# Kernel optimization log

Measured on AMD Instinct MI355X. Metric: run time of the kernel, lower is better.

Reference implementation:

```python
import jax, jax.numpy as jnp
import numpy as np

PADDING_IDX = 0
N_WORDS = 256  # max_n_words (num_segments for pooling)


def _segment_mean(h, wid):
    # h: (S, H), wid: (S,) int32 in [0, N_WORDS). Mean-pool subwords per word.
    sums = jax.ops.segment_sum(h, wid, num_segments=N_WORDS)          # (W, H)
    cnt = jax.ops.segment_sum(jnp.ones(wid.shape, h.dtype), wid,
                              num_segments=N_WORDS)                    # (W,)
    # words with no subwords -> zero vector (matches pad_sequence padding_value=0.0)
    return jnp.where(cnt[:, None] > 0, sums / jnp.maximum(cnt, 1.0)[:, None], 0.0)


def setup_inputs() -> dict:
    key = jax.random.key(0)
    k1, k2, k3, k4, k5 = jax.random.split(key, 5)
    B, S, H, W, V = 16, 512, 768, N_WORDS, 32000
    hidden_states = jax.random.normal(k1, (B, S, H), dtype=jnp.float32)
    word_ids = jnp.sort(jax.random.randint(k2, (B, S), 0, W), axis=-1).astype(jnp.int32)
    targets = jax.random.randint(k3, (B, W), 0, V).astype(jnp.int32)
    W_cls = jax.random.normal(k4, (H, V), dtype=jnp.float32) * 0.02
    b_cls = jax.random.normal(k5, (V,), dtype=jnp.float32) * 0.02
    return {"hidden_states": hidden_states, "word_ids": word_ids,
            "targets": targets, "W_cls": W_cls, "b_cls": b_cls}


def reference(hidden_states, word_ids, targets, W_cls, b_cls):
    # subword -> word mean pooling (fused scatter-mean, vmapped over batch)
    pooled = jax.vmap(_segment_mean)(hidden_states, word_ids)      # (B, W, H)
    # dropout is identity in eval / deterministic mode
    logits = jnp.einsum('bwh,hv->bwv', pooled, W_cls) + b_cls       # (B, W, V)
    # cross-entropy with ignore_index=PADDING_IDX, mean reduction
    logp = jax.nn.log_softmax(logits, axis=-1)
    tgt_logp = jnp.take_along_axis(logp, targets[..., None].astype(jnp.int32), axis=-1)[..., 0]
    mask = (targets != PADDING_IDX).astype(logits.dtype)
    loss = -(tgt_logp * mask).sum() / jnp.maximum(mask.sum(), 1.0)
    return loss
```

## Files before the change

### kernel.cpp

```cpp
#include <hip/hip_runtime.h>
#include <math.h>

#define BB 16
#define SS 512
#define HH 768
#define WW 256
#define VV 32000
#define NROWS (BB*WW)
#define NCHUNK 500
#define BM 128
#define BN 128
#define BK 64
#define NKT (HH/BK)
#define NMT (NROWS/BM)
#define NVT (VV/BN)
#define NWG (NMT*NVT)
#define WSCALE 64.0f
#define WISCALE (1.0f/64.0f)

typedef __attribute__((ext_vector_type(4))) float f32x4;

#define GLOAD16(g, l) __builtin_amdgcn_global_load_lds( \
    (const __attribute__((address_space(1))) void*)(g), \
    (__attribute__((address_space(3))) void*)(l), 16, 0, 0)

__device__ __forceinline__ unsigned int pk4_fp8(float a0, float a1, float a2, float a3) {
    int r = __builtin_amdgcn_cvt_pk_fp8_f32(a0, a1, 0, false);
    r = __builtin_amdgcn_cvt_pk_fp8_f32(a2, a3, r, true);
    return (unsigned int)r;
}

__global__ __launch_bounds__(256) void pool_kernel(
    const float* __restrict__ h, const int* __restrict__ wid,
    unsigned int* __restrict__ pooled32)
{
    int blk = blockIdx.x;
    int b = blk >> 8;
    int w = blk & 255;
    int tid = threadIdx.x;
    __shared__ int s_wid[SS];
    for (int i = tid; i < SS; i += 256) s_wid[i] = wid[b*SS + i];
    __syncthreads();
    int lo = 0, hi = SS;
    while (lo < hi) { int mid = (lo + hi) >> 1; if (s_wid[mid] < w) lo = mid + 1; else hi = mid; }
    int start = lo;
    hi = SS;
    while (lo < hi) { int mid = (lo + hi) >> 1; if (s_wid[mid] <= w) lo = mid + 1; else hi = mid; }
    int end = lo;
    int cnt = end - start;

    if (tid < 192) {
        float4 a = {0.f, 0.f, 0.f, 0.f};
        const float* hb = h + (size_t)b*SS*HH;
        for (int s = start; s < end; ++s) {
            float4 r = *(const float4*)&hb[(size_t)s*HH + tid*4];
            a.x += r.x; a.y += r.y; a.z += r.z; a.w += r.w;
        }
        float inv = (cnt > 0) ? (1.0f / (float)cnt) : 0.0f;
        int p = (blk >> 3) & 1;
        pooled32[blk*192 + (tid ^ (p << 1))] = pk4_fp8(a.x*inv, a.y*inv, a.z*inv, a.w*inv);
    }
}

__global__ __launch_bounds__(256) void wt_kernel(
    const float* __restrict__ Wc, unsigned char* __restrict__ Wt)
{
    const int v0 = blockIdx.x * 64;
    const int k0 = blockIdx.y * 64;
    const int t = threadIdx.x;
    __shared__ float S[64][65];
    #pragma unroll
    for (int j = 0; j < 4; ++j) {
        int idx = t + j*256;
        int kr = idx >> 4;
        int vs = idx & 15;
        float4 f = *(const float4*)&Wc[(size_t)(k0+kr)*VV + v0 + vs*4];
        S[kr][vs*4+0] = f.x; S[kr][vs*4+1] = f.y;
        S[kr][vs*4+2] = f.z; S[kr][vs*4+3] = f.w;
    }
    __syncthreads();
    #pragma unroll
    for (int j = 0; j < 2; ++j) {
        int idx = t + j*256;
        int vi = idx >> 3;
        int ks = idx & 7;
        float f[8];
        #pragma unroll
        for (int i = 0; i < 8; ++i) f[i] = S[ks*8+i][vi] * WSCALE;
        uint2 o;
        o.x = pk4_fp8(f[0], f[1], f[2], f[3]);
        o.y = pk4_fp8(f[4], f[5], f[6], f[7]);
        int p = (vi >> 3) & 1;
        *(uint2*)&Wt[(size_t)(v0+vi)*HH + k0 + (ks ^ p)*8] = o;
    }
}

__global__ __launch_bounds__(256, 4) void logits_kernel(
    const unsigned char* __restrict__ Pb, const unsigned char* __restrict__ Wt,
    const float* __restrict__ bc, const int* __restrict__ targets,
    float* __restrict__ pmax, float* __restrict__ psum,
    float* __restrict__ tlogit)
{
    __shared__ unsigned char Alds[2][BM*BK];
    __shared__ unsigned char Blds[2][BN*BK];

    const int id = blockIdx.x;
    const int wg = (id & 7) * (NWG/8) + (id >> 3);
    const int mt = wg % NMT;
    const int vt = wg / NMT;

    const int t = threadIdx.x;
    const int w = t >> 6;
    const int lane = t & 63;
    const int r16 = lane & 15;
    const int kb = lane >> 4;
    const int wr = w >> 1;
    const int wc = w & 1;
    const int row0 = mt * BM;
    const int v0 = vt * BN;

    const int rr = lane >> 2;
    const int sg = (lane & 3) ^ ((rr >> 1) & 3);

    #define STAGE(BUF, KT) do {                                                   \
        const int k0_ = (KT) * BK;                                                \
        _Pragma("unroll")                                                         \
        for (int j_ = 0; j_ < 2; ++j_) {                                          \
            int ca_ = w*2 + j_;                                                   \
            GLOAD16(Pb + (size_t)(row0 + ca_*16 + rr)*HH + k0_ + sg*16,           \
                    &Alds[BUF][ca_*1024]);                                        \
            GLOAD16(Wt + (size_t)(v0 + ca_*16 + rr)*HH + k0_ + sg*16,             \
                    &Blds[BUF][ca_*1024]);                                        \
        }                                                                         \
    } while (0)

    f32x4 acc[4][4];
    #pragma unroll
    for (int mf = 0; mf < 4; ++mf)
        #pragma unroll
        for (int nf = 0; nf < 4; ++nf)
            acc[mf][nf] = (f32x4){0.f, 0.f, 0.f, 0.f};

    STAGE(0, 0);
    __syncthreads();

    const int swz2 = (r16 >> 1) & 3;
    const int swz3 = (r16 >> 3) & 1;

    for (int kt = 0; kt < NKT; ++kt) {
        const int buf = kt & 1;
        if (kt + 1 < NKT) STAGE(buf ^ 1, kt + 1);

        long af[4][2], bfv[4][2];
        #pragma unroll
        for (int ks = 0; ks < 2; ++ks) {
            const int idx8 = ks*4 + kb;
            const int off = (((idx8 >> 1) ^ swz2) << 4) | (((idx8 & 1) ^ swz3) << 3);
            #pragma unroll
            for (int mf = 0; mf < 4; ++mf)
                af[mf][ks] = *(const long*)&Alds[buf][(wr*64 + mf*16 + r16)*BK + off];
            #pragma unroll
            for (int nf = 0; nf < 4; ++nf)
                bfv[nf][ks] = *(const long*)&Blds[buf][(wc*64 + nf*16 + r16)*BK + off];
        }

        __builtin_amdgcn_s_setprio(1);
        #pragma unroll
        for (int ks = 0; ks < 2; ++ks)
            #pragma unroll
            for (int mf = 0; mf < 4; ++mf)
                #pragma unroll
                for (int nf = 0; nf < 4; ++nf)
                    acc[mf][nf] = __builtin_amdgcn_mfma_f32_16x16x32_fp8_fp8(
                        af[mf][ks], bfv[nf][ks], acc[mf][nf], 0, 0, 0);
        __builtin_amdgcn_s_setprio(0);

        __syncthreads();
    }

    const int cchunk = vt*2 + wc;
    float bias[4];
    #pragma unroll
    for (int nf = 0; nf < 4; ++nf) bias[nf] = bc[v0 + wc*64 + nf*16 + r16];

    #pragma unroll
    for (int mf = 0; mf < 4; ++mf) {
        #pragma unroll
        for (int j = 0; j < 4; ++j) {
            const int row = row0 + wr*64 + mf*16 + kb*4 + j;
            float v[4]; float mx = -INFINITY;
            #pragma unroll
            for (int nf = 0; nf < 4; ++nf) {
                v[nf] = acc[mf][nf][j]*WISCALE + bias[nf];
                mx = fmaxf(mx, v[nf]);
            }
            #pragma unroll
            for (int off = 1; off < 16; off <<= 1)
                mx = fmaxf(mx, __shfl_xor(mx, off, 16));
            float se = 0.f;
            #pragma unroll
            for (int nf = 0; nf < 4; ++nf) se += __expf(v[nf] - mx);
            #pragma unroll
            for (int off = 1; off < 16; off <<= 1)
                se += __shfl_xor(se, off, 16);
            if (r16 == 0) {
                pmax[(size_t)row*NCHUNK + cchunk] = mx;
                psum[(size_t)row*NCHUNK + cchunk] = se;
            }
            int tg = targets[row];
            int base = v0 + wc*64 + r16;
            #pragma unroll
            for (int nf = 0; nf < 4; ++nf)
                if (tg == base + nf*16) tlogit[row] = v[nf];
        }
    }
}

__global__ __launch_bounds__(256) void reduce_kernel(
    const float* __restrict__ pmax, const float* __restrict__ psum,
    const float* __restrict__ tlogit, const int* __restrict__ targets,
    float* __restrict__ rowloss)
{
    const int row = blockIdx.x;
    const int tid = threadIdx.x;
    float m0 = (tid       < NCHUNK) ? pmax[(size_t)row*NCHUNK + tid]       : -INFINITY;
    float m1 = (tid + 256 < NCHUNK) ? pmax[(size_t)row*NCHUNK + tid + 256] : -INFINITY;
    float mw = fmaxf(m0, m1);
    #pragma unroll
    for (int off = 1; off < 64; off <<= 1)
        mw = fmaxf(mw, __shfl_xor(mw, off));
    __shared__ float smax[4];
    __shared__ float ssum[4];
    const int wave = tid >> 6;
    if ((tid & 63) == 0) smax[wave] = mw;
    __syncthreads();
    float mx = fmaxf(fmaxf(smax[0], smax[1]), fmaxf(smax[2], smax[3]));
    float s = 0.f;
    if (tid       < NCHUNK) s += psum[(size_t)row*NCHUNK + tid]       * __expf(m0 - mx);
    if (tid + 256 < NCHUNK) s += psum[(size_t)row*NCHUNK + tid + 256] * __expf(m1 - mx);
    #pragma unroll
    for (int off = 1; off < 64; off <<= 1)
        s += __shfl_xor(s, off);
    if ((tid & 63) == 0) ssum[wave] = s;
    __syncthreads();
    if (tid == 0) {
        float st = ssum[0] + ssum[1] + ssum[2] + ssum[3];
        float lse = mx + logf(st);
        int tg = targets[row];
        rowloss[row] = (tg != 0) ? (lse - tlogit[row]) : 0.0f;
    }
}

__global__ __launch_bounds__(256) void finalize_kernel(
    const float* __restrict__ rowloss, const int* __restrict__ targets,
    float* __restrict__ out)
{
    const int tid = threadIdx.x;
    float s = 0.f; float c = 0.f;
    for (int i = tid; i < NROWS; i += 256) {
        s += rowloss[i];
        c += (targets[i] != 0) ? 1.0f : 0.0f;
    }
    #pragma unroll
    for (int off = 1; off < 64; off <<= 1) {
        s += __shfl_xor(s, off);
        c += __shfl_xor(c, off);
    }
    __shared__ float ss[4], sc[4];
    const int wave = tid >> 6;
    if ((tid & 63) == 0) { ss[wave] = s; sc[wave] = c; }
    __syncthreads();
    if (tid == 0) {
        float st = ss[0]+ss[1]+ss[2]+ss[3];
        float ct = sc[0]+sc[1]+sc[2]+sc[3];
        out[0] = st / fmaxf(ct, 1.0f);
    }
}

extern "C" void kernel_launch(void* const* d_in, const int* in_sizes, int n_in,
                              void* d_out, int out_size, void* d_ws, size_t ws_size,
                              hipStream_t stream) {
    const float* h       = (const float*)d_in[0];
    const int*   wid     = (const int*)  d_in[1];
    const int*   targets = (const int*)  d_in[2];
    const float* Wc      = (const float*)d_in[3];
    const float* bc      = (const float*)d_in[4];
    float* out = (float*)d_out;

    unsigned char* pooled = (unsigned char*)d_ws;
    unsigned char* Wt     = pooled + (size_t)NROWS*HH;
    float* pmax  = (float*)(Wt + (size_t)HH*VV);
    float* psum  = pmax + (size_t)NROWS*NCHUNK;
    float* tlog  = psum + (size_t)NROWS*NCHUNK;
    float* rowl  = tlog + NROWS;

    pool_kernel<<<NROWS, 256, 0, stream>>>(h, wid, (unsigned int*)pooled);
    wt_kernel<<<dim3(VV/64, HH/64), 256, 0, stream>>>(Wc, Wt);
    logits_kernel<<<NWG, 256, 0, stream>>>(
        pooled, Wt, bc, targets, pmax, psum, tlog);
    reduce_kernel<<<NROWS, 256, 0, stream>>>(pmax, psum, tlog, targets, rowl);
    finalize_kernel<<<1, 256, 0, stream>>>(rowl, targets, out);
}
```

Measured before the change: 224.8 us.

## Make logits GEMM persistent with cross-tile prefetch and merge prep kernels

Merges the pooling and weight-transpose/FP8-quantize kernels into one launch, with blocks chosen by index. Converts the logits GEMM to a persistent kernel of 1024 blocks, each looping over its XCD's tiles. Each block prefetches the first two K-slices of its next tile during the final K-step and the softmax epilogue. This hides the tile prologue and cuts launch and tail costs, but adds register pressure and relies on 1024 blocks all being resident at once.

```diff
diff --git a/kernel.cpp b/kernel.cpp
--- a/kernel.cpp
+++ b/kernel.cpp
@@ -15,6 +15,8 @@
 #define NMT (NROWS/BM)
 #define NVT (VV/BN)
 #define NWG (NMT*NVT)
+#define NPX (NWG/8)
+#define NBLK 1024
 #define WSCALE 64.0f
 #define WISCALE (1.0f/64.0f)
 
@@ -30,68 +32,68 @@
     return (unsigned int)r;
 }
 
-__global__ __launch_bounds__(256) void pool_kernel(
+__global__ __launch_bounds__(256) void prep_kernel(
     const float* __restrict__ h, const int* __restrict__ wid,
-    unsigned int* __restrict__ pooled32)
-{
-    int blk = blockIdx.x;
-    int b = blk >> 8;
-    int w = blk & 255;
-    int tid = threadIdx.x;
-    __shared__ int s_wid[SS];
-    for (int i = tid; i < SS; i += 256) s_wid[i] = wid[b*SS + i];
-    __syncthreads();
-    int lo = 0, hi = SS;
-    while (lo < hi) { int mid = (lo + hi) >> 1; if (s_wid[mid] < w) lo = mid + 1; else hi = mid; }
-    int start = lo;
-    hi = SS;
-    while (lo < hi) { int mid = (lo + hi) >> 1; if (s_wid[mid] <= w) lo = mid + 1; else hi = mid; }
-    int end = lo;
-    int cnt = end - start;
-
-    if (tid < 192) {
-        float4 a = {0.f, 0.f, 0.f, 0.f};
-        const float* hb = h + (size_t)b*SS*HH;
-        for (int s = start; s < end; ++s) {
-            float4 r = *(const float4*)&hb[(size_t)s*HH + tid*4];
-            a.x += r.x; a.y += r.y; a.z += r.z; a.w += r.w;
-        }
-        float inv = (cnt > 0) ? (1.0f / (float)cnt) : 0.0f;
-        int p = (blk >> 3) & 1;
-        pooled32[blk*192 + (tid ^ (p << 1))] = pk4_fp8(a.x*inv, a.y*inv, a.z*inv, a.w*inv);
-    }
-}
-
-__global__ __launch_bounds__(256) void wt_kernel(
+    unsigned int* __restrict__ pooled32,
     const float* __restrict__ Wc, unsigned char* __restrict__ Wt)
 {
-    const int v0 = blockIdx.x * 64;
-    const int k0 = blockIdx.y * 64;
-    const int t = threadIdx.x;
+    __shared__ int s_wid[SS];
     __shared__ float S[64][65];
-    #pragma unroll
-    for (int j = 0; j < 4; ++j) {
-        int idx = t + j*256;
-        int kr = idx >> 4;
-        int vs = idx & 15;
-        float4 f = *(const float4*)&Wc[(size_t)(k0+kr)*VV + v0 + vs*4];
-        S[kr][vs*4+0] = f.x; S[kr][vs*4+1] = f.y;
-        S[kr][vs*4+2] = f.z; S[kr][vs*4+3] = f.w;
-    }
-    __syncthreads();
-    #pragma unroll
-    for (int j = 0; j < 2; ++j) {
-        int idx = t + j*256;
-        int vi = idx >> 3;
-        int ks = idx & 7;
-        float f[8];
-        #pragma unroll
-        for (int i = 0; i < 8; ++i) f[i] = S[ks*8+i][vi] * WSCALE;
-        uint2 o;
-        o.x = pk4_fp8(f[0], f[1], f[2], f[3]);
-        o.y = pk4_fp8(f[4], f[5], f[6], f[7]);
-        int p = (vi >> 3) & 1;
-        *(uint2*)&Wt[(size_t)(v0+vi)*HH + k0 + (ks ^ p)*8] = o;
+    const int tid = threadIdx.x;
+
+    if (blockIdx.x < NROWS) {
+        int blk = blockIdx.x;
+        int b = blk >> 8;
+        int w = blk & 255;
+        for (int i = tid; i < SS; i += 256) s_wid[i] = wid[b*SS + i];
+        __syncthreads();
+        int lo = 0, hi = SS;
+        while (lo < hi) { int mid = (lo + hi) >> 1; if (s_wid[mid] < w) lo = mid + 1; else hi = mid; }
+        int start = lo;
+        hi = SS;
+        while (lo < hi) { int mid = (lo + hi) >> 1; if (s_wid[mid] <= w) lo = mid + 1; else hi = mid; }
+        int end = lo;
+        int cnt = end - start;
+
+        if (tid < 192) {
+            float4 a = {0.f, 0.f, 0.f, 0.f};
+            const float* hb = h + (size_t)b*SS*HH;
+            for (int s = start; s < end; ++s) {
+                float4 r = *(const float4*)&hb[(size_t)s*HH + tid*4];
+                a.x += r.x; a.y += r.y; a.z += r.z; a.w += r.w;
+            }
+            float inv = (cnt > 0) ? (1.0f / (float)cnt) : 0.0f;
+            int p = (blk >> 3) & 1;
+            pooled32[blk*192 + (tid ^ (p << 1))] = pk4_fp8(a.x*inv, a.y*inv, a.z*inv, a.w*inv);
+        }
+    } else {
+        int idx = blockIdx.x - NROWS;
+        const int v0 = (idx % (VV/64)) * 64;
+        const int k0 = (idx / (VV/64)) * 64;
+        #pragma unroll
+        for (int j = 0; j < 4; ++j) {
+            int ix = tid + j*256;
+            int kr = ix >> 4;
+            int vs = ix & 15;
+            float4 f = *(const float4*)&Wc[(size_t)(k0+kr)*VV + v0 + vs*4];
+            S[kr][vs*4+0] = f.x; S[kr][vs*4+1] = f.y;
+            S[kr][vs*4+2] = f.z; S[kr][vs*4+3] = f.w;
+        }
+        __syncthreads();
+        #pragma unroll
+        for (int j = 0; j < 2; ++j) {
+            int ix = tid + j*256;
+            int vi = ix >> 3;
+            int ks = ix & 7;
+            float f[8];
+            #pragma unroll
+            for (int i = 0; i < 8; ++i) f[i] = S[ks*8+i][vi] * WSCALE;
+            uint2 o;
+            o.x = pk4_fp8(f[0], f[1], f[2], f[3]);
+            o.y = pk4_fp8(f[4], f[5], f[6], f[7]);
+            int p = (vi >> 3) & 1;
+            *(uint2*)&Wt[(size_t)(v0+vi)*HH + k0 + (ks ^ p)*8] = o;
+        }
     }
 }
 
@@ -104,10 +106,9 @@
     __shared__ unsigned char Alds[2][BM*BK];
     __shared__ unsigned char Blds[2][BN*BK];
 
-    const int id = blockIdx.x;
-    const int wg = (id & 7) * (NWG/8) + (id >> 3);
-    const int mt = wg % NMT;
-    const int vt = wg / NMT;
+    const int bid = blockIdx.x;
+    const int xcd = bid & 7;
+    const int lid = bid >> 3;
 
     const int t = threadIdx.x;
     const int w = t >> 6;
@@ -116,102 +117,128 @@
     const int kb = lane >> 4;
     const int wr = w >> 1;
     const int wc = w & 1;
-    const int row0 = mt * BM;
-    const int v0 = vt * BN;
 
     const int rr = lane >> 2;
     const int sg = (lane & 3) ^ ((rr >> 1) & 3);
 
-    #define STAGE(BUF, KT) do {                                                   \
+    #define STAGEP(BUF, R0, V0, KT) do {                                          \
         const int k0_ = (KT) * BK;                                                \
         _Pragma("unroll")                                                         \
         for (int j_ = 0; j_ < 2; ++j_) {                                          \
             int ca_ = w*2 + j_;                                                   \
-            GLOAD16(Pb + (size_t)(row0 + ca_*16 + rr)*HH + k0_ + sg*16,           \
+            GLOAD16(Pb + (size_t)((R0) + ca_*16 + rr)*HH + k0_ + sg*16,           \
                     &Alds[BUF][ca_*1024]);                                        \
-            GLOAD16(Wt + (size_t)(v0 + ca_*16 + rr)*HH + k0_ + sg*16,             \
+            GLOAD16(Wt + (size_t)((V0) + ca_*16 + rr)*HH + k0_ + sg*16,           \
                     &Blds[BUF][ca_*1024]);                                        \
         }                                                                         \
     } while (0)
 
-    f32x4 acc[4][4];
-    #pragma unroll
-    for (int mf = 0; mf < 4; ++mf)
-        #pragma unroll
-        for (int nf = 0; nf < 4; ++nf)
-            acc[mf][nf] = (f32x4){0.f, 0.f, 0.f, 0.f};
-
-    STAGE(0, 0);
-    __syncthreads();
-
     const int swz2 = (r16 >> 1) & 3;
     const int swz3 = (r16 >> 3) & 1;
 
-    for (int kt = 0; kt < NKT; ++kt) {
-        const int buf = kt & 1;
-        if (kt + 1 < NKT) STAGE(buf ^ 1, kt + 1);
-
-        long af[4][2], bfv[4][2];
-        #pragma unroll
-        for (int ks = 0; ks < 2; ++ks) {
-            const int idx8 = ks*4 + kb;
-            const int off = (((idx8 >> 1) ^ swz2) << 4) | (((idx8 & 1) ^ swz3) << 3);
-            #pragma unroll
-            for (int mf = 0; mf < 4; ++mf)
-                af[mf][ks] = *(const long*)&Alds[buf][(wr*64 + mf*16 + r16)*BK + off];
+    {
+        const int wg0 = xcd*NPX + lid;
+        const int r0 = (wg0 & (NMT-1)) * BM;
+        const int c0 = (wg0 >> 5) * BN;
+        STAGEP(0, r0, c0, 0);
+        STAGEP(1, r0, c0, 1);
+        __syncthreads();
+    }
+
+    for (int wci = lid; wci < NPX; wci += (NBLK/8)) {
+        const int wg = xcd*NPX + wci;
+        const int mt = wg & (NMT-1);
+        const int vt = wg >> 5;
+        const int row0 = mt * BM;
+        const int v0 = vt * BN;
+
+        const int wciN = wci + (NBLK/8);
+        const bool hasNext = (wciN < NPX);
+        const int wgN = xcd*NPX + (hasNext ? wciN : 0);
+        const int row0N = (wgN & (NMT-1)) * BM;
+        const int v0N = (wgN >> 5) * BN;
+
+        f32x4 acc[4][4];
+        #pragma unroll
+        for (int mf = 0; mf < 4; ++mf)
             #pragma unroll
             for (int nf = 0; nf < 4; ++nf)
-                bfv[nf][ks] = *(const long*)&Blds[buf][(wc*64 + nf*16 + r16)*BK + off];
-        }
-
-        __builtin_amdgcn_s_setprio(1);
-        #pragma unroll
-        for (int ks = 0; ks < 2; ++ks)
-            #pragma unroll
-            for (int mf = 0; mf < 4; ++mf)
+                acc[mf][nf] = (f32x4){0.f, 0.f, 0.f, 0.f};
+
+        #pragma unroll
+        for (int kt = 0; kt < NKT; ++kt) {
+            const int buf = kt & 1;
+
+            if (kt >= 1 && kt + 1 < NKT) {
+                STAGEP(buf ^ 1, row0, v0, kt + 1);
+            } else if (kt == NKT - 1) {
+                if (hasNext) STAGEP(0, row0N, v0N, 0);
+            }
+
+            long af[4][2], bfv[4][2];
+            #pragma unroll
+            for (int ks = 0; ks < 2; ++ks) {
+                const int idx8 = ks*4 + kb;
+                const int off = (((idx8 >> 1) ^ swz2) << 4) | (((idx8 & 1) ^ swz3) << 3);
+                #pragma unroll
+                for (int mf = 0; mf < 4; ++mf)
+                    af[mf][ks] = *(const long*)&Alds[buf][(wr*64 + mf*16 + r16)*BK + off];
                 #pragma unroll
                 for (int nf = 0; nf < 4; ++nf)
-                    acc[mf][nf] = __builtin_amdgcn_mfma_f32_16x16x32_fp8_fp8(
-                        af[mf][ks], bfv[nf][ks], acc[mf][nf], 0, 0, 0);
-        __builtin_amdgcn_s_setprio(0);
-
-        __syncthreads();
-    }
-
-    const int cchunk = vt*2 + wc;
-    float bias[4];
-    #pragma unroll
-    for (int nf = 0; nf < 4; ++nf) bias[nf] = bc[v0 + wc*64 + nf*16 + r16];
-
-    #pragma unroll
-    for (int mf = 0; mf < 4; ++mf) {
-        #pragma unroll
-        for (int j = 0; j < 4; ++j) {
-            const int row = row0 + wr*64 + mf*16 + kb*4 + j;
-            float v[4]; float mx = -INFINITY;
-            #pragma unroll
-            for (int nf = 0; nf < 4; ++nf) {
-                v[nf] = acc[mf][nf][j]*WISCALE + bias[nf];
-                mx = fmaxf(mx, v[nf]);
+                    bfv[nf][ks] = *(const long*)&Blds[buf][(wc*64 + nf*16 + r16)*BK + off];
             }
-            #pragma unroll
-            for (int off = 1; off < 16; off <<= 1)
-                mx = fmaxf(mx, __shfl_xor(mx, off, 16));
-            float se = 0.f;
-            #pragma unroll
-            for (int nf = 0; nf < 4; ++nf) se += __expf(v[nf] - mx);
-            #pragma unroll
-            for (int off = 1; off < 16; off <<= 1)
-                se += __shfl_xor(se, off, 16);
-            if (r16 == 0) {
-                pmax[(size_t)row*NCHUNK + cchunk] = mx;
-                psum[(size_t)row*NCHUNK + cchunk] = se;
+
+            __builtin_amdgcn_s_setprio(1);
+            #pragma unroll
+            for (int ks = 0; ks < 2; ++ks)
+                #pragma unroll
+                for (int mf = 0; mf < 4; ++mf)
+                    #pragma unroll
+                    for (int nf = 0; nf < 4; ++nf)
+                        acc[mf][nf] = __builtin_amdgcn_mfma_f32_16x16x32_fp8_fp8(
+                            af[mf][ks], bfv[nf][ks], acc[mf][nf], 0, 0, 0);
+            __builtin_amdgcn_s_setprio(0);
+
+            __syncthreads();
+        }
+
+        if (hasNext) STAGEP(1, row0N, v0N, 1);
+
+        const int cchunk = vt*2 + wc;
+        float bias[4];
+        #pragma unroll
+        for (int nf = 0; nf < 4; ++nf) bias[nf] = bc[v0 + wc*64 + nf*16 + r16];
+
+        #pragma unroll
+        for (int mf = 0; mf < 4; ++mf) {
+            #pragma unroll
+            for (int j = 0; j < 4; ++j) {
+                const int row = row0 + wr*64 + mf*16 + kb*4 + j;
+                float v[4]; float mx = -INFINITY;
+                #pragma unroll
+                for (int nf = 0; nf < 4; ++nf) {
+                    v[nf] = acc[mf][nf][j]*WISCALE + bias[nf];
+                    mx = fmaxf(mx, v[nf]);
+                }
+                #pragma unroll
+                for (int off = 1; off < 16; off <<= 1)
+                    mx = fmaxf(mx, __shfl_xor(mx, off, 16));
+                float se = 0.f;
+                #pragma unroll
+                for (int nf = 0; nf < 4; ++nf) se += __expf(v[nf] - mx);
+                #pragma unroll
+                for (int off = 1; off < 16; off <<= 1)
+                    se += __shfl_xor(se, off, 16);
+                if (r16 == 0) {
+                    pmax[(size_t)row*NCHUNK + cchunk] = mx;
+                    psum[(size_t)row*NCHUNK + cchunk] = se;
+                }
+                int tg = targets[row];
+                int base = v0 + wc*64 + r16;
+                #pragma unroll
+                for (int nf = 0; nf < 4; ++nf)
+                    if (tg == base + nf*16) tlogit[row] = v[nf];
             }
-            int tg = targets[row];
-            int base = v0 + wc*64 + r16;
-            #pragma unroll
-            for (int nf = 0; nf < 4; ++nf)
-                if (tg == base + nf*16) tlogit[row] = v[nf];
         }
     }
 }
@@ -294,9 +321,9 @@
     float* tlog  = psum + (size_t)NROWS*NCHUNK;
     float* rowl  = tlog + NROWS;
 
-    pool_kernel<<<NROWS, 256, 0, stream>>>(h, wid, (unsigned int*)pooled);
-    wt_kernel<<<dim3(VV/64, HH/64), 256, 0, stream>>>(Wc, Wt);
-    logits_kernel<<<NWG, 256, 0, stream>>>(
+    prep_kernel<<<NROWS + (VV/64)*(HH/64), 256, 0, stream>>>(
+        h, wid, (unsigned int*)pooled, Wc, Wt);
+    logits_kernel<<<NBLK, 256, 0, stream>>>(
         pooled, Wt, bc, targets, pmax, psum, tlog);
     reduce_kernel<<<NROWS, 256, 0, stream>>>(pmax, psum, tlog, targets, rowl);
     finalize_kernel<<<1, 256, 0, stream>>>(rowl, targets, out);
```

After: 267.1 us. 18.8% more time.
